# Kernel optimization log

Hardware: AMD Instinct MI355X
Metric: run time of the kernel (lower is better)

Reference implementation:

```python
import jax, jax.numpy as jnp
import numpy as np

TOP_K = 2


def setup_inputs() -> dict:
    key = jax.random.key(0)
    k1, k2 = jax.random.split(key)
    hidden_states = jax.random.normal(k1, (4, 8192, 4096), dtype=jnp.float32)
    # xavier_uniform for Linear(4096 -> 64): bound = sqrt(6/(fan_in+fan_out))
    bound = float(np.sqrt(6.0 / (4096 + 64)))
    gate_w = jax.random.uniform(k2, (64, 4096), dtype=jnp.float32, minval=-bound, maxval=bound)
    return {"hidden_states": hidden_states, "gate_w": gate_w}


def reference(hidden_states, gate_w):
    # Flatten [B, S, H] -> [T, H]
    H = hidden_states.shape[-1]
    x = hidden_states.reshape(-1, H)
    # Gate projection: [T, H] @ [H, E] -> [T, E]
    router_logits = jnp.einsum('th,eh->te', x, gate_w)
    # Top-k expert selection (eval mode: no noise)
    top_k_logits, top_k_indices = jax.lax.top_k(router_logits, TOP_K)
    # Normalize selected weights with a softmax over the k logits
    top_k_weights = jax.nn.softmax(top_k_logits, axis=-1)
    return top_k_weights, top_k_indices, router_logits
```

## Files before the change

kernel.cpp:

```cpp
#include <hip/hip_runtime.h>


#define NT   256
#define TT   32768
#define HD   4096
#define NE   64
#define BMT  64
#define BKT  64
#define NKT  (HD / BKT)

typedef __attribute__((ext_vector_type(8))) short bf16x8;
typedef __attribute__((ext_vector_type(4))) float f32x4;

#define MFMA __builtin_amdgcn_mfma_f32_16x16x32_bf16

__device__ __forceinline__ unsigned rne_bf16(float f) {
  unsigned u = __float_as_uint(f);
  return (u + 0x7fffu + ((u >> 16) & 1u)) >> 16;
}

__device__ __forceinline__ void split8(float4 a, float4 b,
                                       uint4& o0, uint4& o1, uint4& o2) {
  float f[8] = {a.x, a.y, a.z, a.w, b.x, b.y, b.z, b.w};
  unsigned h0[8], h1[8], h2[8];
#pragma unroll
  for (int j = 0; j < 8; ++j) {
    float x = f[j];
    unsigned u0 = rne_bf16(x);
    float g0 = __uint_as_float(u0 << 16);
    float r1 = x - g0;
    unsigned u1 = rne_bf16(r1);
    float g1 = __uint_as_float(u1 << 16);
    float r2 = r1 - g1;
    h0[j] = u0; h1[j] = u1; h2[j] = rne_bf16(r2);
  }
  o0 = make_uint4(h0[0]|(h0[1]<<16), h0[2]|(h0[3]<<16), h0[4]|(h0[5]<<16), h0[6]|(h0[7]<<16));
  o1 = make_uint4(h1[0]|(h1[1]<<16), h1[2]|(h1[3]<<16), h1[4]|(h1[5]<<16), h1[6]|(h1[7]<<16));
  o2 = make_uint4(h2[0]|(h2[1]<<16), h2[2]|(h2[3]<<16), h2[4]|(h2[5]<<16), h2[6]|(h2[7]<<16));
}


__global__ __launch_bounds__(NT, 2)
void topk_router_kernel(const float* __restrict__ A, const float* __restrict__ W,
                        float* __restrict__ outw, float* __restrict__ outi,
                        float* __restrict__ outl) {
  __shared__ __align__(16) unsigned char smem[49152];

  const int tid  = threadIdx.x;
  const int bm   = blockIdx.x;
  const int lane = tid & 63;
  const int wid  = tid >> 6;
  const int wr   = wid >> 1;
  const int wc   = wid & 1;
  const int l15  = lane & 15;
  const int lg   = lane >> 4;

  const int a_r = tid >> 2;
  const int a_c = (tid & 3) << 4;

  const float* aptr = A + ((size_t)(bm * BMT + a_r)) * HD + a_c;
  const float* bptr = W + ((size_t)a_r) * HD + a_c;

  const unsigned sw  = ((unsigned)(a_r & 7)) << 4;
  const unsigned cw0 = (unsigned)(a_r * 128) + (((unsigned)(a_c * 2 +  0)) ^ sw);
  const unsigned cw1 = (unsigned)(a_r * 128) + (((unsigned)(a_c * 2 + 16)) ^ sw);

  float4 av0, av1, av2, av3, bv0, bv1, bv2, bv3;

  f32x4 acc00 = {0.f, 0.f, 0.f, 0.f};
  f32x4 acc01 = {0.f, 0.f, 0.f, 0.f};
  f32x4 acc10 = {0.f, 0.f, 0.f, 0.f};
  f32x4 acc11 = {0.f, 0.f, 0.f, 0.f};

  auto stage = [&](int k0) {
    const float4* ap = (const float4*)(aptr + k0);
    av0 = ap[0]; av1 = ap[1]; av2 = ap[2]; av3 = ap[3];
    const float4* bp = (const float4*)(bptr + k0);
    bv0 = bp[0]; bv1 = bp[1]; bv2 = bp[2]; bv3 = bp[3];
  };

  auto convwrite = [&]() {
    uint4 o0, o1, o2;
    split8(av0, av1, o0, o1, o2);
    *(uint4*)(smem +     0 + cw0) = o0;
    *(uint4*)(smem +  8192 + cw0) = o1;
    *(uint4*)(smem + 16384 + cw0) = o2;
    split8(av2, av3, o0, o1, o2);
    *(uint4*)(smem +     0 + cw1) = o0;
    *(uint4*)(smem +  8192 + cw1) = o1;
    *(uint4*)(smem + 16384 + cw1) = o2;
    split8(bv0, bv1, o0, o1, o2);
    *(uint4*)(smem + 24576 + cw0) = o0;
    *(uint4*)(smem + 32768 + cw0) = o1;
    *(uint4*)(smem + 40960 + cw0) = o2;
    split8(bv2, bv3, o0, o1, o2);
    *(uint4*)(smem + 24576 + cw1) = o0;
    *(uint4*)(smem + 32768 + cw1) = o1;
    *(uint4*)(smem + 40960 + cw1) = o2;
  };

  auto compute = [&]() {
#pragma unroll
    for (int ks = 0; ks < 2; ++ks) {
      bf16x8 a0m0, a0m1, a1m0, a1m1, a2m0, a2m1;
      bf16x8 b0n0, b0n1, b1n0, b1n1, b2n0, b2n1;
      const unsigned kb = (unsigned)(ks * 64 + lg * 16);
#define LDA(SI, MI, DST) { \
      int row = wr * 32 + (MI) * 16 + l15; \
      DST = *(const bf16x8*)(smem + (SI) * 8192 + row * 128 + (kb ^ (((unsigned)(row & 7)) << 4))); }
#define LDB(SI, NI, DST) { \
      int row = wc * 32 + (NI) * 16 + l15; \
      DST = *(const bf16x8*)(smem + 24576 + (SI) * 8192 + row * 128 + (kb ^ (((unsigned)(row & 7)) << 4))); }
      LDA(0, 0, a0m0) LDA(0, 1, a0m1)
      LDA(1, 0, a1m0) LDA(1, 1, a1m1)
      LDA(2, 0, a2m0) LDA(2, 1, a2m1)
      LDB(0, 0, b0n0) LDB(0, 1, b0n1)
      LDB(1, 0, b1n0) LDB(1, 1, b1n1)
      LDB(2, 0, b2n0) LDB(2, 1, b2n1)
#undef LDA
#undef LDB
#define PROD(AI, BI) \
      acc00 = MFMA(a##AI##m0, b##BI##n0, acc00, 0, 0, 0); \
      acc01 = MFMA(a##AI##m0, b##BI##n1, acc01, 0, 0, 0); \
      acc10 = MFMA(a##AI##m1, b##BI##n0, acc10, 0, 0, 0); \
      acc11 = MFMA(a##AI##m1, b##BI##n1, acc11, 0, 0, 0);
      PROD(0, 2) PROD(1, 1) PROD(2, 0) PROD(0, 1) PROD(1, 0) PROD(0, 0)
#undef PROD
    }
  };

  stage(0);
  convwrite();
  __syncthreads();

  for (int kt = 0; kt < NKT; ++kt) {
    const bool more = (kt + 1 < NKT);
    if (more) stage((kt + 1) * BKT);
    compute();
    __syncthreads();
    if (more) convwrite();
    __syncthreads();
  }

  const int t0 = bm * BMT;
  float* lf = (float*)smem;

#define EPI(MI, NI, ACC) \
  { _Pragma("unroll") \
    for (int r = 0; r < 4; ++r) { \
      int tl = wr * 32 + (MI) * 16 + lg * 4 + r; \
      int e  = wc * 32 + (NI) * 16 + l15; \
      float v = ACC[r]; \
      outl[(size_t)(t0 + tl) * NE + e] = v; \
      lf[tl * 65 + e] = v; \
    } }
  EPI(0, 0, acc00) EPI(0, 1, acc01) EPI(1, 0, acc10) EPI(1, 1, acc11)
#undef EPI

  __syncthreads();

  if (tid < BMT) {
    const int t = tid;
    float m1 = -1e30f, m2 = -1e30f;
    int i1 = 0, i2 = 0;
#pragma unroll
    for (int e = 0; e < NE; ++e) {
      float v = lf[t * 65 + e];
      if (v > m1)      { m2 = m1; i2 = i1; m1 = v; i1 = e; }
      else if (v > m2) { m2 = v; i2 = e; }
    }
    float e2  = expf(m2 - m1);
    float inv = 1.0f / (1.0f + e2);
    outw[(size_t)(t0 + t) * 2 + 0] = inv;
    outw[(size_t)(t0 + t) * 2 + 1] = e2 * inv;
    outi[(size_t)(t0 + t) * 2 + 0] = (float)i1;
    outi[(size_t)(t0 + t) * 2 + 1] = (float)i2;
  }
}

extern "C" void kernel_launch(void* const* d_in, const int* in_sizes, int n_in,
                              void* d_out, int out_size, void* d_ws, size_t ws_size,
                              hipStream_t stream) {
  (void)in_sizes; (void)n_in; (void)d_ws; (void)ws_size; (void)out_size;
  const float* A = (const float*)d_in[0];
  const float* W = (const float*)d_in[1];
  float* outw = (float*)d_out;
  float* outi = (float*)d_out + 2 * TT;
  float* outl = (float*)d_out + 4 * TT;

  dim3 grid(TT / BMT);
  dim3 block(NT);
  hipLaunchKernelGGL(topk_router_kernel, grid, block, 0, stream, A, W, outw, outi, outl);
}
```

Before: 203.2 us.

## Double-buffer LDS with two-deep register prefetch and truncating bf16 split

The K tile shrinks to 32 and the 48KB of LDS becomes two 24KB buffers, so converting and writing the next tile overlaps with computing the current one. Global loads are issued two tiles ahead through alternating even/odd register sets, with sched_barriers to keep them in place. The split of fp32 into three bf16 parts now uses truncation instead of round-to-nearest-even, which needs fewer ALU ops. The three-term split is still exact enough, but the residual terms differ slightly from before. There are twice as many loop iterations, and register pressure rises from the extra prefetch set.

```diff
diff --git a/kernel.cpp b/kernel.cpp
--- a/kernel.cpp
+++ b/kernel.cpp
@@ -6,7 +6,7 @@
 #define HD   4096
 #define NE   64
 #define BMT  64
-#define BKT  64
+#define BKT  32
 #define NKT  (HD / BKT)
 
 typedef __attribute__((ext_vector_type(8))) short bf16x8;
@@ -14,29 +14,28 @@
 
 #define MFMA __builtin_amdgcn_mfma_f32_16x16x32_bf16
 
-__device__ __forceinline__ unsigned rne_bf16(float f) {
-  unsigned u = __float_as_uint(f);
-  return (u + 0x7fffu + ((u >> 16) & 1u)) >> 16;
-}
-
-__device__ __forceinline__ void split8(float4 a, float4 b,
-                                       uint4& o0, uint4& o1, uint4& o2) {
+__device__ __forceinline__ void tsplit8(float4 a, float4 b,
+                                        uint4& o0, uint4& o1, uint4& o2) {
   float f[8] = {a.x, a.y, a.z, a.w, b.x, b.y, b.z, b.w};
-  unsigned h0[8], h1[8], h2[8];
+  unsigned p0[4], p1[4], p2[4];
 #pragma unroll
-  for (int j = 0; j < 8; ++j) {
-    float x = f[j];
-    unsigned u0 = rne_bf16(x);
-    float g0 = __uint_as_float(u0 << 16);
-    float r1 = x - g0;
-    unsigned u1 = rne_bf16(r1);
-    float g1 = __uint_as_float(u1 << 16);
-    float r2 = r1 - g1;
-    h0[j] = u0; h1[j] = u1; h2[j] = rne_bf16(r2);
+  for (int j = 0; j < 4; ++j) {
+    float x0 = f[2 * j], x1 = f[2 * j + 1];
+    unsigned u0 = __float_as_uint(x0) & 0xffff0000u;
+    unsigned u1 = __float_as_uint(x1) & 0xffff0000u;
+    float r0 = x0 - __uint_as_float(u0);
+    float r1 = x1 - __uint_as_float(u1);
+    unsigned v0 = __float_as_uint(r0) & 0xffff0000u;
+    unsigned v1 = __float_as_uint(r1) & 0xffff0000u;
+    float s0 = r0 - __uint_as_float(v0);
+    float s1 = r1 - __uint_as_float(v1);
+    p0[j] = (u0 >> 16) | u1;
+    p1[j] = (v0 >> 16) | v1;
+    p2[j] = (__float_as_uint(s0) >> 16) | (__float_as_uint(s1) & 0xffff0000u);
   }
-  o0 = make_uint4(h0[0]|(h0[1]<<16), h0[2]|(h0[3]<<16), h0[4]|(h0[5]<<16), h0[6]|(h0[7]<<16));
-  o1 = make_uint4(h1[0]|(h1[1]<<16), h1[2]|(h1[3]<<16), h1[4]|(h1[5]<<16), h1[6]|(h1[7]<<16));
-  o2 = make_uint4(h2[0]|(h2[1]<<16), h2[2]|(h2[3]<<16), h2[4]|(h2[5]<<16), h2[6]|(h2[7]<<16));
+  o0 = make_uint4(p0[0], p0[1], p0[2], p0[3]);
+  o1 = make_uint4(p1[0], p1[1], p1[2], p1[3]);
+  o2 = make_uint4(p2[0], p2[1], p2[2], p2[3]);
 }
 
 
@@ -55,90 +54,83 @@
   const int l15  = lane & 15;
   const int lg   = lane >> 4;
 
-  const int a_r = tid >> 2;
-  const int a_c = (tid & 3) << 4;
+  const int s_r  = tid >> 2;
+  const int s_cb = (tid & 3) << 3;
 
-  const float* aptr = A + ((size_t)(bm * BMT + a_r)) * HD + a_c;
-  const float* bptr = W + ((size_t)a_r) * HD + a_c;
+  const float* aball = A + (size_t)(bm * BMT + s_r) * HD + s_cb;
+  const float* bball = W + (size_t)s_r * HD + s_cb;
 
-  const unsigned sw  = ((unsigned)(a_r & 7)) << 4;
-  const unsigned cw0 = (unsigned)(a_r * 128) + (((unsigned)(a_c * 2 +  0)) ^ sw);
-  const unsigned cw1 = (unsigned)(a_r * 128) + (((unsigned)(a_c * 2 + 16)) ^ sw);
+  const unsigned wswz  = ((unsigned)((s_r >> 1) & 3)) << 4;
+  const unsigned wbyte = (unsigned)(s_r * 64) + (((unsigned)(s_cb * 2)) ^ wswz);
 
-  float4 av0, av1, av2, av3, bv0, bv1, bv2, bv3;
+  f32x4 acc00 = {0.f,0.f,0.f,0.f}, acc01 = {0.f,0.f,0.f,0.f};
+  f32x4 acc10 = {0.f,0.f,0.f,0.f}, acc11 = {0.f,0.f,0.f,0.f};
 
-  f32x4 acc00 = {0.f, 0.f, 0.f, 0.f};
-  f32x4 acc01 = {0.f, 0.f, 0.f, 0.f};
-  f32x4 acc10 = {0.f, 0.f, 0.f, 0.f};
-  f32x4 acc11 = {0.f, 0.f, 0.f, 0.f};
+  float4 aE0, aE1, bE0, bE1;
+  float4 aO0, aO1, bO0, bO1;
 
-  auto stage = [&](int k0) {
-    const float4* ap = (const float4*)(aptr + k0);
-    av0 = ap[0]; av1 = ap[1]; av2 = ap[2]; av3 = ap[3];
-    const float4* bp = (const float4*)(bptr + k0);
-    bv0 = bp[0]; bv1 = bp[1]; bv2 = bp[2]; bv3 = bp[3];
-  };
+#define LOADS(T, A0, A1, B0, B1) { \
+    const float4* ap = (const float4*)(aball + (size_t)(T) * BKT); \
+    A0 = ap[0]; A1 = ap[1]; \
+    const float4* bp = (const float4*)(bball + (size_t)(T) * BKT); \
+    B0 = bp[0]; B1 = bp[1]; }
 
-  auto convwrite = [&]() {
-    uint4 o0, o1, o2;
-    split8(av0, av1, o0, o1, o2);
-    *(uint4*)(smem +     0 + cw0) = o0;
-    *(uint4*)(smem +  8192 + cw0) = o1;
-    *(uint4*)(smem + 16384 + cw0) = o2;
-    split8(av2, av3, o0, o1, o2);
-    *(uint4*)(smem +     0 + cw1) = o0;
-    *(uint4*)(smem +  8192 + cw1) = o1;
-    *(uint4*)(smem + 16384 + cw1) = o2;
-    split8(bv0, bv1, o0, o1, o2);
-    *(uint4*)(smem + 24576 + cw0) = o0;
-    *(uint4*)(smem + 32768 + cw0) = o1;
-    *(uint4*)(smem + 40960 + cw0) = o2;
-    split8(bv2, bv3, o0, o1, o2);
-    *(uint4*)(smem + 24576 + cw1) = o0;
-    *(uint4*)(smem + 32768 + cw1) = o1;
-    *(uint4*)(smem + 40960 + cw1) = o2;
-  };
+#define CONVW(BB, A0, A1, B0, B1) { \
+    uint4 o0, o1, o2; \
+    tsplit8(A0, A1, o0, o1, o2); \
+    *(uint4*)(smem + (BB) +     0 + wbyte) = o0; \
+    *(uint4*)(smem + (BB) +  4096 + wbyte) = o1; \
+    *(uint4*)(smem + (BB) +  8192 + wbyte) = o2; \
+    tsplit8(B0, B1, o0, o1, o2); \
+    *(uint4*)(smem + (BB) + 12288 + wbyte) = o0; \
+    *(uint4*)(smem + (BB) + 16384 + wbyte) = o1; \
+    *(uint4*)(smem + (BB) + 20480 + wbyte) = o2; }
 
-  auto compute = [&]() {
-#pragma unroll
-    for (int ks = 0; ks < 2; ++ks) {
-      bf16x8 a0m0, a0m1, a1m0, a1m1, a2m0, a2m1;
-      bf16x8 b0n0, b0n1, b1n0, b1n1, b2n0, b2n1;
-      const unsigned kb = (unsigned)(ks * 64 + lg * 16);
+  auto compute = [&](int bb) {
+    bf16x8 a0m0, a0m1, a1m0, a1m1, a2m0, a2m1;
+    bf16x8 b0n0, b0n1, b1n0, b1n1, b2n0, b2n1;
+    const unsigned kb = (unsigned)(lg * 16);
 #define LDA(SI, MI, DST) { \
-      int row = wr * 32 + (MI) * 16 + l15; \
-      DST = *(const bf16x8*)(smem + (SI) * 8192 + row * 128 + (kb ^ (((unsigned)(row & 7)) << 4))); }
+    int row = wr * 32 + (MI) * 16 + l15; \
+    DST = *(const bf16x8*)(smem + bb + (SI) * 4096 + row * 64 + \
+          (kb ^ ((((unsigned)row >> 1) & 3) << 4))); }
 #define LDB(SI, NI, DST) { \
-      int row = wc * 32 + (NI) * 16 + l15; \
-      DST = *(const bf16x8*)(smem + 24576 + (SI) * 8192 + row * 128 + (kb ^ (((unsigned)(row & 7)) << 4))); }
-      LDA(0, 0, a0m0) LDA(0, 1, a0m1)
-      LDA(1, 0, a1m0) LDA(1, 1, a1m1)
-      LDA(2, 0, a2m0) LDA(2, 1, a2m1)
-      LDB(0, 0, b0n0) LDB(0, 1, b0n1)
-      LDB(1, 0, b1n0) LDB(1, 1, b1n1)
-      LDB(2, 0, b2n0) LDB(2, 1, b2n1)
+    int row = wc * 32 + (NI) * 16 + l15; \
+    DST = *(const bf16x8*)(smem + bb + 12288 + (SI) * 4096 + row * 64 + \
+          (kb ^ ((((unsigned)row >> 1) & 3) << 4))); }
+    LDA(0, 0, a0m0) LDA(0, 1, a0m1)
+    LDA(1, 0, a1m0) LDA(1, 1, a1m1)
+    LDA(2, 0, a2m0) LDA(2, 1, a2m1)
+    LDB(0, 0, b0n0) LDB(0, 1, b0n1)
+    LDB(1, 0, b1n0) LDB(1, 1, b1n1)
+    LDB(2, 0, b2n0) LDB(2, 1, b2n1)
 #undef LDA
 #undef LDB
 #define PROD(AI, BI) \
-      acc00 = MFMA(a##AI##m0, b##BI##n0, acc00, 0, 0, 0); \
-      acc01 = MFMA(a##AI##m0, b##BI##n1, acc01, 0, 0, 0); \
-      acc10 = MFMA(a##AI##m1, b##BI##n0, acc10, 0, 0, 0); \
-      acc11 = MFMA(a##AI##m1, b##BI##n1, acc11, 0, 0, 0);
-      PROD(0, 2) PROD(1, 1) PROD(2, 0) PROD(0, 1) PROD(1, 0) PROD(0, 0)
+    acc00 = MFMA(a##AI##m0, b##BI##n0, acc00, 0, 0, 0); \
+    acc01 = MFMA(a##AI##m0, b##BI##n1, acc01, 0, 0, 0); \
+    acc10 = MFMA(a##AI##m1, b##BI##n0, acc10, 0, 0, 0); \
+    acc11 = MFMA(a##AI##m1, b##BI##n1, acc11, 0, 0, 0);
+    PROD(0, 2) PROD(1, 1) PROD(2, 0) PROD(0, 1) PROD(1, 0) PROD(0, 0)
 #undef PROD
-    }
   };
 
-  stage(0);
-  convwrite();
+  LOADS(0, aE0, aE1, bE0, bE1)
+  LOADS(1, aO0, aO1, bO0, bO1)
+  CONVW(0, aE0, aE1, bE0, bE1)
   __syncthreads();
 
-  for (int kt = 0; kt < NKT; ++kt) {
-    const bool more = (kt + 1 < NKT);
-    if (more) stage((kt + 1) * BKT);
-    compute();
+#pragma unroll 1
+  for (int kk = 0; kk < NKT; kk += 2) {
+    if (kk + 2 < NKT) { LOADS(kk + 2, aE0, aE1, bE0, bE1) }
+    __builtin_amdgcn_sched_barrier(0);
+    compute(0);
+    CONVW(24576, aO0, aO1, bO0, bO1)
     __syncthreads();
-    if (more) convwrite();
+    if (kk + 3 < NKT) { LOADS(kk + 3, aO0, aO1, bO0, bO1) }
+    __builtin_amdgcn_sched_barrier(0);
+    compute(24576);
+    if (kk + 2 < NKT) { CONVW(0, aE0, aE1, bE0, bE1) }
     __syncthreads();
   }
 
```

Result: faster. 168.5 us (-17.1%).
